# Kernel tuning notes

Hardware: AMD Instinct MI355X
Metric: run time of the kernel (lower is better)

The kernel has to match this reference:

```python
import jax, jax.numpy as jnp
import numpy as np

THRESHOLD = 0.5
NEG_POS_RATIO = 3
CONF_WEIGHT = 1.0
VAR = (0.1, 0.1, 0.2, 0.2)
EPS_LOG = 1e-5


def _center_to_corner(p):
    cx, cy, w, h = p[:, 0], p[:, 1], p[:, 2], p[:, 3]
    return jnp.stack([cx - w / 2, cy - h / 2, cx + w / 2, cy + h / 2], axis=1)


def _iou(gt, pr):  # gt [M,4] corners, pr [P,4] corners -> [M,P]
    lt = jnp.maximum(gt[:, None, :2], pr[None, :, :2])
    rb = jnp.minimum(gt[:, None, 2:], pr[None, :, 2:])
    wh = jnp.clip(rb - lt, 0.0)
    inter = wh[..., 0] * wh[..., 1]
    area_g = (gt[:, 2] - gt[:, 0]) * (gt[:, 3] - gt[:, 1])
    area_p = (pr[:, 2] - pr[:, 0]) * (pr[:, 3] - pr[:, 1])
    return inter / (area_g[:, None] + area_p[None, :] - inter + 1e-10)


def _match_one(gt_boxes, priors_corner):
    # standard SSD matching: per-prior best GT if IoU >= threshold, else -1;
    # each GT additionally claims its best prior.
    iou = _iou(gt_boxes, priors_corner)            # [M,P]
    best_gt = jnp.argmax(iou, axis=0)              # [P]
    best_iou = jnp.max(iou, axis=0)                # [P]
    truth = jnp.where(best_iou >= THRESHOLD, best_gt, -1)
    best_prior = jnp.argmax(iou, axis=1)           # [M]
    truth = truth.at[best_prior].set(jnp.arange(gt_boxes.shape[0]))
    return truth


def _encode(matched_gt, priors):
    # matched_gt [B,P,4] corners, priors [P,4] center form -> [B,P,4]
    g_cx = (matched_gt[..., 0] + matched_gt[..., 2]) / 2
    g_cy = (matched_gt[..., 1] + matched_gt[..., 3]) / 2
    g_w = matched_gt[..., 2] - matched_gt[..., 0]
    g_h = matched_gt[..., 3] - matched_gt[..., 1]
    p_cx, p_cy, p_w, p_h = priors[:, 0], priors[:, 1], priors[:, 2], priors[:, 3]
    enc_cx = (g_cx - p_cx) / (p_w * VAR[0])
    enc_cy = (g_cy - p_cy) / (p_h * VAR[1])
    enc_w = jnp.log(g_w / p_w + EPS_LOG) / VAR[2]
    enc_h = jnp.log(g_h / p_h + EPS_LOG) / VAR[3]
    return jnp.stack([enc_cx, enc_cy, enc_w, enc_h], axis=-1)


def setup_inputs() -> dict:
    key = jax.random.key(0)
    ks = jax.random.split(key, 7)
    B, P, C, M = 64, 8732, 81, 20
    pred_loc = jax.random.normal(ks[0], (B, P, 4), jnp.float32)
    pred_conf = jax.random.normal(ks[1], (B, P, C), jnp.float32)
    # priors in center form (cx, cy, w, h)
    p_c = jax.random.uniform(ks[2], (P, 2), jnp.float32)
    p_wh = jax.random.uniform(ks[3], (P, 2), jnp.float32, minval=0.05, maxval=0.5)
    priors = jnp.concatenate([p_c, p_wh], axis=1)
    # GT boxes in corner form, guaranteed valid (x2>x1, y2>y1)
    g_c = jax.random.uniform(ks[4], (B, M, 2), jnp.float32, minval=0.2, maxval=0.8)
    g_wh = jax.random.uniform(ks[5], (B, M, 2), jnp.float32, minval=0.05, maxval=0.3)
    targets_boxes = jnp.concatenate([g_c - g_wh / 2, g_c + g_wh / 2], axis=-1)
    targets_labels = jax.random.randint(ks[6], (B, M), 1, C, jnp.int32)
    return {"pred_loc": pred_loc, "pred_conf": pred_conf, "priors": priors,
            "targets_boxes": targets_boxes, "targets_labels": targets_labels}


def reference(pred_loc, pred_conf, priors, targets_boxes, targets_labels):
    B, P, C = pred_conf.shape
    priors_corner = _center_to_corner(priors)
    truth = jax.vmap(lambda g: _match_one(g, priors_corner))(targets_boxes)  # [B,P]
    pos_mask = truth != -1
    safe = jnp.maximum(truth, 0)
    matched_gt = jax.vmap(lambda t, s: t[s])(targets_boxes, safe)            # [B,P,4]
    target_conf = jnp.where(pos_mask,
                            jax.vmap(lambda l, s: l[s])(targets_labels, safe), 0)

    # localization loss: smooth-L1 (beta=1), sum over matched priors, / batch
    enc = _encode(matched_gt, priors)
    d = pred_loc - enc
    ad = jnp.abs(d)
    sl1 = jnp.where(ad < 1.0, 0.5 * d * d, ad - 0.5)
    loc_loss = jnp.sum(sl1 * pos_mask[..., None]) / B

    # confidence loss with hard negative mining (3:1, double-argsort rank trick)
    logp = jax.nn.log_softmax(pred_conf, axis=-1)                            # [B,P,C]
    ce = -jnp.take_along_axis(logp, target_conf[..., None], axis=-1)[..., 0]  # [B,P]
    ce_neg = jnp.where(pos_mask, 0.0, ce)
    order = jnp.argsort(-ce_neg, axis=1)
    rank = jnp.argsort(order, axis=1)
    pos_num = jnp.sum(pos_mask, axis=1, keepdims=True)
    neg_num = jnp.minimum(NEG_POS_RATIO * pos_num, P - 1)
    neg_mask = rank < neg_num
    prior_mask = pos_mask | neg_mask
    conf_loss = jnp.sum(ce * prior_mask) / jnp.sum(prior_mask) / B * CONF_WEIGHT
    return (loc_loss, conf_loss)
```

## Files before the change

### kernel.cpp

```cpp
#include <hip/hip_runtime.h>
#include <hip/hip_bf16.h>

#define B_   64
#define P_   8732
#define C_   81
#define M_   20
#define BP_  (B_*P_)
#define CEB  128
#define CETH 512
#define NV   (CEB*C_/4)
#define NCH  9
#define SBLK 1024

__global__ __launch_bounds__(256) void iou_kernel(
    const float* __restrict__ priors, const float* __restrict__ tboxes,
    int* __restrict__ truth, unsigned long long* __restrict__ bestc)
{
    const int b = blockIdx.y;
    const int tid = threadIdx.x;
    __shared__ float s_gt[M_][4];
    __shared__ float s_ga[M_];
    __shared__ float s_red[M_][4];
    __shared__ int   s_redp[M_][4];

    if (tid < M_*4) ((float*)s_gt)[tid] = tboxes[b*M_*4 + tid];
    __syncthreads();
    if (tid < M_) s_ga[tid] = (s_gt[tid][2]-s_gt[tid][0]) * (s_gt[tid][3]-s_gt[tid][1]);
    __syncthreads();

    float lb[M_]; int lp[M_];
    #pragma unroll
    for (int m=0;m<M_;++m){ lb[m] = -1.0f; lp[m] = 0x7FFFFFFF; }

    const float4* pr4 = (const float4*)priors;
    const int p0 = blockIdx.x * 1024;
    const int pend = min(p0 + 1024, P_);
    for (int p = p0 + tid; p < pend; p += 256) {
        float4 pc = pr4[p];
        float px0 = pc.x - pc.z*0.5f, py0 = pc.y - pc.w*0.5f;
        float px1 = pc.x + pc.z*0.5f, py1 = pc.y + pc.w*0.5f;
        float pa = pc.z * pc.w;
        float best = -1.0f; int bg = 0;
        #pragma unroll
        for (int m=0;m<M_;++m){
            float ix0 = fmaxf(s_gt[m][0], px0);
            float iy0 = fmaxf(s_gt[m][1], py0);
            float ix1 = fminf(s_gt[m][2], px1);
            float iy1 = fminf(s_gt[m][3], py1);
            float iw = fmaxf(ix1-ix0, 0.f), ih = fmaxf(iy1-iy0, 0.f);
            float inter = iw*ih;
            float iou = inter / (s_ga[m] + pa - inter + 1e-10f);
            if (iou > best) { best = iou; bg = m; }
            if (iou > lb[m]) { lb[m] = iou; lp[m] = p; }
        }
        truth[(size_t)b*P_ + p] = (best >= 0.5f) ? bg : -1;
    }

    const int lane = tid & 63, wid = tid >> 6;
    #pragma unroll
    for (int m=0;m<M_;++m){
        float v = lb[m]; int ip = lp[m];
        for (int off=32; off; off>>=1){
            float ov = __shfl_down(v, off); int op = __shfl_down(ip, off);
            if (ov > v || (ov == v && op < ip)) { v = ov; ip = op; }
        }
        if (lane == 0) { s_red[m][wid] = v; s_redp[m][wid] = ip; }
    }
    __syncthreads();
    if (tid < M_) {
        const int m = tid;
        float v = s_red[m][0]; int ip = s_redp[m][0];
        for (int w=1; w<4; ++w){
            float ov = s_red[m][w]; int op = s_redp[m][w];
            if (ov > v || (ov == v && op < ip)) { v = ov; ip = op; }
        }
        bestc[(b*M_ + m)*NCH + blockIdx.x] =
            ((unsigned long long)__float_as_uint(v) << 32) | (unsigned)(P_ - 1 - ip);
    }
}

__global__ void override_kernel(const unsigned long long* __restrict__ bestc,
                                int* __restrict__ truth,
                                int* __restrict__ pos_cnt, float* __restrict__ pos_sum,
                                float* __restrict__ accums, int* __restrict__ done)
{
    const int tid = threadIdx.x;
    __shared__ int s_bp[B_*M_];

    if (tid < B_) { pos_cnt[tid] = 0; pos_sum[tid] = 0.f; }
    if (tid < 3)  accums[tid] = 0.f;
    if (tid == 3) *done = 0;

    for (int pair = tid; pair < B_*M_; pair += 256) {
        const unsigned long long* src = &bestc[pair*NCH];
        unsigned long long best = src[0];
        #pragma unroll
        for (int c = 1; c < NCH; ++c) { unsigned long long k = src[c]; if (k > best) best = k; }
        s_bp[pair] = P_ - 1 - (int)(unsigned)(best & 0xFFFFFFFFu);
    }
    __syncthreads();
    if (tid < B_) {
        int* trow = truth + (size_t)tid * P_;
        for (int m = 0; m < M_; ++m) trow[s_bp[tid*M_ + m]] = m;
    }
}

__global__ __launch_bounds__(CETH) void ce_loc_kernel(
    const float* __restrict__ pred_conf, const float* __restrict__ pred_loc,
    const float* __restrict__ priors, const float* __restrict__ tboxes,
    const int* __restrict__ tlabels, const int* __restrict__ truth,
    float* __restrict__ ce_neg, int* __restrict__ pos_cnt,
    float* __restrict__ pos_sum, float* __restrict__ accums)
{
    __shared__ float sc[CEB * C_];
    __shared__ int   s_pos[2];
    __shared__ float s_psum[2];
    __shared__ float s_loc[CETH/64];
    const int tid = threadIdx.x;
    const int base = blockIdx.x * CEB;
    const int b0 = base / P_;

    const float4* src4 = (const float4*)(pred_conf + (size_t)base * C_);
    float4* dst4 = (float4*)sc;
#if __has_builtin(__builtin_amdgcn_global_load_lds)
    #pragma unroll
    for (int k = 0; k < NV / CETH; ++k) {
        const int i = tid + k * CETH;
        __builtin_amdgcn_global_load_lds(
            (const __attribute__((address_space(1))) void*)(src4 + i),
            (__attribute__((address_space(3))) void*)(dst4 + i), 16, 0, 0);
    }
    if (tid < NV - (NV / CETH) * CETH) {
        const int i = (NV / CETH) * CETH + tid;
        __builtin_amdgcn_global_load_lds(
            (const __attribute__((address_space(1))) void*)(src4 + i),
            (__attribute__((address_space(3))) void*)(dst4 + i), 16, 0, 0);
    }
#else
    for (int i = tid; i < NV; i += CETH) dst4[i] = src4[i];
#endif
    if (tid < 2) { s_pos[tid] = 0; s_psum[tid] = 0.f; }
    __syncthreads();

    const int r = tid >> 2;
    const int q = tid & 3;
    const float* row = &sc[r * C_];
    const int c0 = q * 20 + (q > 0 ? 1 : 0);
    const int cn = (q == 0) ? 21 : 20;
    float mx = -1e30f;
    for (int c = 0; c < cn; ++c) mx = fmaxf(mx, row[c0 + c]);
    mx = fmaxf(mx, __shfl_xor(mx, 1));
    mx = fmaxf(mx, __shfl_xor(mx, 2));
    float s = 0.f;
    for (int c = 0; c < cn; ++c) s += __expf(row[c0 + c] - mx);
    s += __shfl_xor(s, 1);
    s += __shfl_xor(s, 2);

    float locacc = 0.f;
    if (q == 0) {
        const int bp = base + r;
        const int b = bp / P_;
        const int p = bp - b * P_;
        const int t = truth[bp];
        const int cls = (t >= 0) ? tlabels[b*M_ + t] : 0;
        const float ce = mx + __logf(s) - row[cls];
        if (t >= 0) {
            atomicAdd(&s_pos[b - b0], 1);
            atomicAdd(&s_psum[b - b0], ce);
            ce_neg[bp] = 0.f;
            float4 pc = ((const float4*)priors)[p];
            float4 g  = ((const float4*)tboxes)[b*M_ + t];
            float gcx = (g.x+g.z)*0.5f, gcy = (g.y+g.w)*0.5f;
            float gw = g.z - g.x, gh = g.w - g.y;
            float e0 = (gcx - pc.x) / (pc.z * 0.1f);
            float e1 = (gcy - pc.y) / (pc.w * 0.1f);
            float e2 = __logf(gw / pc.z + 1e-5f) * 5.0f;
            float e3 = __logf(gh / pc.w + 1e-5f) * 5.0f;
            float4 pl = ((const float4*)pred_loc)[bp];
            float d0 = pl.x-e0, d1 = pl.y-e1, d2 = pl.z-e2, d3 = pl.w-e3;
            float a0 = fabsf(d0), a1 = fabsf(d1), a2 = fabsf(d2), a3 = fabsf(d3);
            locacc = (a0<1.f ? 0.5f*d0*d0 : a0-0.5f)
                   + (a1<1.f ? 0.5f*d1*d1 : a1-0.5f)
                   + (a2<1.f ? 0.5f*d2*d2 : a2-0.5f)
                   + (a3<1.f ? 0.5f*d3*d3 : a3-0.5f);
        } else {
            ce_neg[bp] = ce;
        }
    }
    for (int off=32; off; off>>=1) locacc += __shfl_down(locacc, off);
    if ((tid & 63) == 0) s_loc[tid>>6] = locacc;
    __syncthreads();
    if (tid == 0) {
        float a = 0.f;
        #pragma unroll
        for (int w = 0; w < CETH/64; ++w) a += s_loc[w];
        if (a != 0.f) atomicAdd(&accums[0], a);
    }
    if (tid < 2) {
        const int br = b0 + tid;
        if (br < B_ && s_pos[tid] > 0) {
            atomicAdd(&pos_cnt[br], s_pos[tid]);
            atomicAdd(&pos_sum[br], s_psum[tid]);
        }
    }
}

__global__ __launch_bounds__(SBLK) void select_kernel(
    const float* __restrict__ ce_neg, const int* __restrict__ pos_cnt,
    const float* __restrict__ pos_sum, float* __restrict__ accums,
    int* __restrict__ done, float* __restrict__ out)
{
    const int b = blockIdx.x; const int tid = threadIdx.x;
    const int lane = tid & 63;
    __shared__ float cl[P_];
    __shared__ unsigned hist[256];
    __shared__ unsigned s_sel, s_prefix, s_remk, s_cntgt;
    __shared__ float s_r1[SBLK/64];
    __shared__ int s_last;

    const float* cerow = ce_neg + (size_t)b * P_;
    if (tid < 256) hist[tid] = 0u;
    if (tid == 0) s_sel = 0u;
    __syncthreads();

    for (int i = tid; i < P_; i += SBLK) {
        const unsigned bin = __float_as_uint(cerow[i]) >> 24;
        unsigned long long todo = __ballot(1);
        while (todo) {
            const int src = (int)__ffsll(todo) - 1;
            const unsigned lead = __shfl(bin, src);
            const unsigned long long mset = __ballot(bin == lead);
            if (lane == src) atomicAdd(&hist[lead], (unsigned)__popcll(mset));
            todo &= ~mset;
        }
    }
    __syncthreads();
    const int pos = pos_cnt[b];
    const unsigned k = (unsigned)min(3 * pos, P_ - 1);
    if (tid == 0) {
        unsigned acc = 0, chosen = 0;
        for (int bin = 255; bin >= 0; --bin) {
            const unsigned c = hist[bin];
            if (acc + c >= k) { chosen = (unsigned)bin; break; }
            acc += c;
        }
        s_prefix = chosen << 24; s_remk = k - acc; s_cntgt = acc;
    }
    __syncthreads();
    const unsigned c3 = s_prefix >> 24;

    float gsum = 0.f;
    for (int i = tid; i < P_; i += SBLK) {
        const float v = cerow[i];
        const unsigned byt = __float_as_uint(v) >> 24;
        if (byt > c3) gsum += v;
        const bool pred = (byt == c3);
        const unsigned long long mset = __ballot(pred);
        if (pred) {
            const int leader = (int)__ffsll(mset) - 1;
            unsigned bse;
            if (lane == leader) bse = atomicAdd(&s_sel, (unsigned)__popcll(mset));
            bse = __shfl(bse, leader);
            cl[bse + __popcll(mset & ((1ull << lane) - 1ull))] = v;
        }
    }
    __syncthreads();
    const int L = (int)s_sel;

    for (int pass = 2; pass >= 0; --pass) {
        if (tid < 256) hist[tid] = 0u;
        __syncthreads();
        const unsigned prefix = s_prefix;
        const int shift = pass * 8;
        const unsigned pmask = 0xFFFFFFFFu << (shift + 8);
        for (int i = tid; i < L; i += SBLK) {
            const unsigned u = __float_as_uint(cl[i]);
            if ((u & pmask) == prefix) atomicAdd(&hist[(u >> shift) & 0xFFu], 1u);
        }
        __syncthreads();
        if (tid == 0) {
            unsigned remk = s_remk, acc = 0, chosen = 0;
            for (int bin = 255; bin >= 0; --bin) {
                const unsigned c = hist[bin];
                if (acc + c >= remk) { chosen = (unsigned)bin; break; }
                acc += c;
            }
            s_cntgt += acc; s_remk = remk - acc; s_prefix = prefix | (chosen << shift);
        }
        __syncthreads();
    }

    const unsigned Tbits = s_prefix;
    const float T = __uint_as_float(Tbits);
    float sgt = gsum;
    for (int i = tid; i < L; i += SBLK) {
        const float v = cl[i];
        if (__float_as_uint(v) > Tbits) sgt += v;
    }
    for (int off=32; off; off>>=1) sgt += __shfl_down(sgt, off);
    if (lane == 0) s_r1[tid>>6] = sgt;
    __syncthreads();
    if (tid == 0) {
        float a = 0.f;
        #pragma unroll
        for (int w = 0; w < SBLK/64; ++w) a += s_r1[w];
        const unsigned sel_eq = s_remk;
        float neg_sum, mc;
        if (Tbits != 0u) { neg_sum = a + (float)sel_eq * T; mc = (float)(pos + (int)k); }
        else             { neg_sum = a;                     mc = (float)(pos + (int)s_cntgt); }
        atomicAdd(&accums[1], pos_sum[b] + neg_sum);
        atomicAdd(&accums[2], mc);
        __threadfence();
        const int old = atomicAdd(done, 1);
        s_last = (old == B_ - 1);
    }
    __syncthreads();
    if (tid == 0 && s_last) {
        const float l  = atomicAdd(&accums[0], 0.f);
        const float cs = atomicAdd(&accums[1], 0.f);
        const float mn = atomicAdd(&accums[2], 0.f);
        out[0] = l / (float)B_;
        out[1] = cs / mn / (float)B_;
    }
}

extern "C" void kernel_launch(void* const* d_in, const int* in_sizes, int n_in,
                              void* d_out, int out_size, void* d_ws, size_t ws_size,
                              hipStream_t stream) {
    (void)in_sizes; (void)n_in; (void)out_size; (void)ws_size;
    const float* pred_loc  = (const float*)d_in[0];
    const float* pred_conf = (const float*)d_in[1];
    const float* priors    = (const float*)d_in[2];
    const float* tboxes    = (const float*)d_in[3];
    const int*   tlabels   = (const int*)d_in[4];
    float* out = (float*)d_out;

    char* ws = (char*)d_ws;
    int*   truth  = (int*)ws;
    float* ce_neg = (float*)(ws + (size_t)BP_ * 4);
    unsigned long long* bestc = (unsigned long long*)(ws + (size_t)BP_ * 8);
    char* tail = ws + (size_t)BP_ * 8 + (size_t)B_*M_*NCH*8;
    int*   pos_cnt = (int*)tail;
    float* pos_sum = (float*)(tail + B_*4);
    float* accums  = (float*)(tail + B_*8);
    int*   done    = (int*)(tail + B_*8 + 12);

    iou_kernel<<<dim3(NCH, B_), 256, 0, stream>>>(priors, tboxes, truth, bestc);
    override_kernel<<<1, 256, 0, stream>>>(bestc, truth, pos_cnt, pos_sum, accums, done);
    ce_loc_kernel<<<BP_ / CEB, CETH, 0, stream>>>(pred_conf, pred_loc, priors, tboxes,
                                                  tlabels, truth, ce_neg, pos_cnt, pos_sum, accums);
    select_kernel<<<B_, SBLK, 0, stream>>>(ce_neg, pos_cnt, pos_sum, accums, done, out);
}
```

Baseline: 158.2 us.

## Fold best-prior override into CE kernel and shrink CE block size

Result: slower. 188.0 us (+18.9%).

```diff
diff --git a/kernel.cpp b/kernel.cpp
--- a/kernel.cpp
+++ b/kernel.cpp
@@ -6,18 +6,27 @@
 #define C_   81
 #define M_   20
 #define BP_  (B_*P_)
-#define CEB  128
-#define CETH 512
+#define CEB  64
+#define CETH 256
 #define NV   (CEB*C_/4)
 #define NCH  9
 #define SBLK 1024
 
 __global__ __launch_bounds__(256) void iou_kernel(
     const float* __restrict__ priors, const float* __restrict__ tboxes,
-    int* __restrict__ truth, unsigned long long* __restrict__ bestc)
+    int* __restrict__ truth, unsigned long long* __restrict__ bestc,
+    int* __restrict__ pos_cnt, float* __restrict__ pos_sum,
+    float* __restrict__ accums, int* __restrict__ done)
 {
     const int b = blockIdx.y;
     const int tid = threadIdx.x;
+
+    if (blockIdx.x == 0 && b == 0) {
+        if (tid < B_) { pos_cnt[tid] = 0; pos_sum[tid] = 0.f; }
+        if (tid >= B_ && tid < B_ + 3) accums[tid - B_] = 0.f;
+        if (tid == B_ + 3) *done = 0;
+    }
+
     __shared__ float s_gt[M_][4];
     __shared__ float s_ga[M_];
     __shared__ float s_red[M_][4];
@@ -79,40 +88,16 @@
     }
 }
 
-__global__ void override_kernel(const unsigned long long* __restrict__ bestc,
-                                int* __restrict__ truth,
-                                int* __restrict__ pos_cnt, float* __restrict__ pos_sum,
-                                float* __restrict__ accums, int* __restrict__ done)
-{
-    const int tid = threadIdx.x;
-    __shared__ int s_bp[B_*M_];
-
-    if (tid < B_) { pos_cnt[tid] = 0; pos_sum[tid] = 0.f; }
-    if (tid < 3)  accums[tid] = 0.f;
-    if (tid == 3) *done = 0;
-
-    for (int pair = tid; pair < B_*M_; pair += 256) {
-        const unsigned long long* src = &bestc[pair*NCH];
-        unsigned long long best = src[0];
-        #pragma unroll
-        for (int c = 1; c < NCH; ++c) { unsigned long long k = src[c]; if (k > best) best = k; }
-        s_bp[pair] = P_ - 1 - (int)(unsigned)(best & 0xFFFFFFFFu);
-    }
-    __syncthreads();
-    if (tid < B_) {
-        int* trow = truth + (size_t)tid * P_;
-        for (int m = 0; m < M_; ++m) trow[s_bp[tid*M_ + m]] = m;
-    }
-}
-
-__global__ __launch_bounds__(CETH) void ce_loc_kernel(
+__global__ __launch_bounds__(CETH, 7) void ce_loc_kernel(
     const float* __restrict__ pred_conf, const float* __restrict__ pred_loc,
     const float* __restrict__ priors, const float* __restrict__ tboxes,
     const int* __restrict__ tlabels, const int* __restrict__ truth,
+    const unsigned long long* __restrict__ bestc,
     float* __restrict__ ce_neg, int* __restrict__ pos_cnt,
     float* __restrict__ pos_sum, float* __restrict__ accums)
 {
     __shared__ float sc[CEB * C_];
+    __shared__ int   s_fp[2][M_];
     __shared__ int   s_pos[2];
     __shared__ float s_psum[2];
     __shared__ float s_loc[CETH/64];
@@ -139,6 +124,20 @@
 #else
     for (int i = tid; i < NV; i += CETH) dst4[i] = src4[i];
 #endif
+
+    if (tid < 2*M_) {
+        const int j = tid / M_, m = tid - j*M_;
+        const int b = b0 + j;
+        int p = -1;
+        if (b < B_) {
+            const unsigned long long* src = &bestc[(b*M_ + m)*NCH];
+            unsigned long long best = src[0];
+            #pragma unroll
+            for (int c = 1; c < NCH; ++c) { unsigned long long kk = src[c]; if (kk > best) best = kk; }
+            p = P_ - 1 - (int)(unsigned)(best & 0xFFFFFFFFu);
+        }
+        s_fp[j][m] = p;
+    }
     if (tid < 2) { s_pos[tid] = 0; s_psum[tid] = 0.f; }
     __syncthreads();
 
@@ -161,12 +160,16 @@
         const int bp = base + r;
         const int b = bp / P_;
         const int p = bp - b * P_;
-        const int t = truth[bp];
+        const int jb = b - b0;
+        int t = truth[bp];
+        #pragma unroll
+        for (int m = 0; m < M_; ++m)
+            if (s_fp[jb][m] == p) t = m;
         const int cls = (t >= 0) ? tlabels[b*M_ + t] : 0;
         const float ce = mx + __logf(s) - row[cls];
         if (t >= 0) {
-            atomicAdd(&s_pos[b - b0], 1);
-            atomicAdd(&s_psum[b - b0], ce);
+            atomicAdd(&s_pos[jb], 1);
+            atomicAdd(&s_psum[jb], ce);
             ce_neg[bp] = 0.f;
             float4 pc = ((const float4*)priors)[p];
             float4 g  = ((const float4*)tboxes)[b*M_ + t];
@@ -345,9 +348,10 @@
     float* accums  = (float*)(tail + B_*8);
     int*   done    = (int*)(tail + B_*8 + 12);
 
-    iou_kernel<<<dim3(NCH, B_), 256, 0, stream>>>(priors, tboxes, truth, bestc);
-    override_kernel<<<1, 256, 0, stream>>>(bestc, truth, pos_cnt, pos_sum, accums, done);
+    iou_kernel<<<dim3(NCH, B_), 256, 0, stream>>>(priors, tboxes, truth, bestc,
+                                                  pos_cnt, pos_sum, accums, done);
     ce_loc_kernel<<<BP_ / CEB, CETH, 0, stream>>>(pred_conf, pred_loc, priors, tboxes,
-                                                  tlabels, truth, ce_neg, pos_cnt, pos_sum, accums);
+                                                  tlabels, truth, bestc,
+                                                  ce_neg, pos_cnt, pos_sum, accums);
     select_kernel<<<B_, SBLK, 0, stream>>>(ce_neg, pos_cnt, pos_sum, accums, done, out);
 }
```
